# Optimization experiments

Hardware: AMD Instinct MI355X
Metric: run time of the kernel (lower is better)

## Reference

```python
import jax, jax.numpy as jnp
import numpy as np
import math

H, D, DFF = 12, 768, 3072
DH = D // H  # 64
B, T = 4, 2048
EPS = 1e-5


def setup_inputs() -> dict:
    key = jax.random.key(0)
    ks = jax.random.split(key, 12)
    randw = lambda k, *d: jax.random.normal(k, d, jnp.float32) / math.sqrt(d[-1])
    return {
        "X": jax.random.normal(ks[0], (B, T, D), jnp.float32),
        "w_q": randw(ks[1], H, DH, D),
        "w_k": randw(ks[2], H, DH, D),
        "w_v": randw(ks[3], H, DH, D),
        "w_o": randw(ks[4], DH * H, D),
        "W1": jax.random.normal(ks[5], (DFF, D), jnp.float32) * 0.02,
        "b1": jnp.zeros((DFF,), jnp.float32),
        "W2": jax.random.normal(ks[6], (D, DFF), jnp.float32) * 0.02,
        "b2": jnp.zeros((D,), jnp.float32),
        "g1": jnp.ones((D,), jnp.float32),
        "be1": jnp.zeros((D,), jnp.float32),
        "g2": jnp.ones((D,), jnp.float32),
        "be2": jnp.zeros((D,), jnp.float32),
    }


def layernorm(x, g, b):
    mu = jnp.mean(x, axis=-1, keepdims=True)
    var = jnp.var(x, axis=-1, keepdims=True)
    return (x - mu) * jax.lax.rsqrt(var + EPS) * g + b


def attention(x, w_q, w_k, w_v, w_o):
    # x: [n,t,c]
    q = jnp.einsum('ntc,hdc->nhtd', x, w_q)
    k = jnp.einsum('ntc,hdc->nhtd', x, w_k)
    v = jnp.einsum('ntc,hdc->nhtd', x, w_v)
    a = jnp.einsum('nhtd,nhsd->nhts', q, k) / math.sqrt(q.shape[3])
    t, s = a.shape[2], a.shape[3]
    forbidden = jnp.arange(t)[:, None] < jnp.arange(s)[None, :]
    a = jnp.where(forbidden, -jnp.inf, a)
    a = jax.nn.softmax(a, axis=3)
    y = jnp.einsum('nhts,nhsd->nthd', a, v).reshape(x.shape[0], t, -1)
    return y @ w_o


def reference(X, w_q, w_k, w_v, w_o, W1, b1, W2, b2, g1, be1, g2, be2):
    X = X + attention(layernorm(X, g1, be1), w_q, w_k, w_v, w_o)
    h = jax.nn.relu(layernorm(X, g2, be2) @ W1.T + b1)
    return X + h @ W2.T + b2
```

## Files before the change

### kernel.cpp

```cpp
#include <hip/hip_runtime.h>
#include <stdint.h>

#define B_   4
#define T_   2048
#define D_   768
#define H_   12
#define DH_  64
#define DFF_ 3072
#define NTOK_ (B_*T_)
#define QKVN_ (3*D_)

typedef unsigned short u16;
typedef __bf16 bf16x8 __attribute__((ext_vector_type(8)));
typedef float  f32x4  __attribute__((ext_vector_type(4)));

__device__ __forceinline__ u16 f2bf(float f) {
  union { float f; unsigned u; } v; v.f = f;
  return (u16)((v.u + 0x7fffu + ((v.u >> 16) & 1u)) >> 16);
}

__device__ __forceinline__ u16 f2bf_ru(float f) {
  union { float f; unsigned u; } v; v.f = f;
  return (u16)((v.u + 0x8000u) >> 16);
}

__device__ __forceinline__ float fast_exp2(float x) {
#if __has_builtin(__builtin_amdgcn_exp2f)
  return __builtin_amdgcn_exp2f(x);
#else
  return exp2f(x);
#endif
}

__device__ __forceinline__ float fast_rcp(float x) {
#if __has_builtin(__builtin_amdgcn_rcpf)
  return __builtin_amdgcn_rcpf(x);
#else
  return 1.0f / x;
#endif
}

__device__ __forceinline__ void gload_lds16(const void* g, void* l) {
  __builtin_amdgcn_global_load_lds(
      (__attribute__((address_space(1))) unsigned int*)(void*)g,
      (__attribute__((address_space(3))) unsigned int*)l, 16, 0, 0);
}

template<bool BIAS, bool RELU, bool RES, bool BF16OUT, bool QSCALE, int BN>
__global__ __launch_bounds__(256) void gemm_bt(
    const u16* __restrict__ A, const u16* __restrict__ Bw,
    const float* __restrict__ bias, const float* __restrict__ res,
    void* __restrict__ outp, int M, int N, int K)
{
  constexpr int NI = BN / 32;
  __shared__ u16 lA[128 * 32];
  __shared__ u16 lB[BN * 32];
  const int tid  = threadIdx.x;
  const int lane = tid & 63;
  const int wave = tid >> 6;
  const int quad = lane >> 4;
  const int l15  = lane & 15;
  const int mBase = blockIdx.x * 128;
  const int nBase = blockIdx.y * BN;
  const int wm = (wave >> 1) * 64;
  const int wn = (wave & 1) * (BN / 2);

  const f32x4 fz = {0.f, 0.f, 0.f, 0.f};
  f32x4 acc[4][NI];
#pragma unroll
  for (int i = 0; i < 4; i++)
#pragma unroll
    for (int j = 0; j < NI; j++) acc[i][j] = fz;

  const int c0 = tid, c1 = tid + 256;
  const u16* gA0 = A  + (size_t)(mBase + (c0 >> 2)) * K + (c0 & 3) * 8;
  const u16* gA1 = A  + (size_t)(mBase + (c1 >> 2)) * K + (c1 & 3) * 8;
  const u16* gB0 = Bw + (size_t)(nBase + (c0 >> 2)) * K + (c0 & 3) * 8;
  const u16* gB1 = (BN == 128)
      ? Bw + (size_t)(nBase + (c1 >> 2)) * K + (c1 & 3) * 8 : nullptr;
  u16* lA0 = lA + c0 * 8; u16* lA1 = lA + c1 * 8;
  u16* lB0 = lB + c0 * 8;
  u16* lB1 = (BN == 128) ? lB + c1 * 8 : nullptr;

  for (int kt = 0; kt < K; kt += 32) {
    gload_lds16(gA0 + kt, lA0);
    gload_lds16(gA1 + kt, lA1);
    gload_lds16(gB0 + kt, lB0);
    if (BN == 128) gload_lds16(gB1 + kt, lB1);
    __syncthreads();
    bf16x8 af[4], bfr[NI];
#pragma unroll
    for (int mi = 0; mi < 4; mi++)
      af[mi] = *(const bf16x8*)(lA + (wm + mi * 16 + l15) * 32 + quad * 8);
#pragma unroll
    for (int ni = 0; ni < NI; ni++)
      bfr[ni] = *(const bf16x8*)(lB + (wn + ni * 16 + l15) * 32 + quad * 8);
#pragma unroll
    for (int mi = 0; mi < 4; mi++)
#pragma unroll
      for (int ni = 0; ni < NI; ni++)
        acc[mi][ni] = __builtin_amdgcn_mfma_f32_16x16x32_bf16(
            af[mi], bfr[ni], acc[mi][ni], 0, 0, 0);
    __syncthreads();
  }

#pragma unroll
  for (int mi = 0; mi < 4; mi++) {
#pragma unroll
    for (int ni = 0; ni < NI; ni++) {
      const int col = nBase + wn + ni * 16 + l15;
      float bv = 0.f;
      if (BIAS) bv = bias[col];
#pragma unroll
      for (int r = 0; r < 4; r++) {
        const int row = mBase + wm + mi * 16 + quad * 4 + r;
        float v = acc[mi][ni][r];
        if (BIAS) v += bv;
        if (RELU) v = fmaxf(v, 0.f);
        if (RES)  v += res[(size_t)row * N + col];
        if (QSCALE && col < D_) v *= 0.180336880f;
        if (BF16OUT) ((u16*)outp)[(size_t)row * N + col] = f2bf(v);
        else        ((float*)outp)[(size_t)row * N + col] = v;
      }
    }
  }
}

__global__ __launch_bounds__(256) void attn_kernel(
    const u16* __restrict__ qkv, const u16* __restrict__ vt, u16* __restrict__ Y)
{
  __shared__ u16 lK[2][64 * 64];
  __shared__ u16 lV[2][64 * 64];
  __shared__ u16 lP[4][16 * 64];
  const int tid  = threadIdx.x;
  const int lane = tid & 63;
  const int wave = tid >> 6;
  const int quad = lane >> 4;
  const int l15  = lane & 15;
  const int qt = 31 - (int)blockIdx.x;
  const int q0 = qt * 64;
  const int h  = blockIdx.y;
  const int b  = blockIdx.z;
  const int qw = q0 + wave * 16;

  bf16x8 qf0, qf1;
  {
    const u16* qp = qkv + (size_t)(b * T_ + qw + l15) * QKVN_ + h * DH_ + quad * 8;
    qf0 = *(const bf16x8*)(qp);
    qf1 = *(const bf16x8*)(qp + 32);
  }

  const f32x4 fz = {0.f, 0.f, 0.f, 0.f};
  f32x4 o[4];
#pragma unroll
  for (int i = 0; i < 4; i++) o[i] = fz;
  float lsum[4] = {0.f, 0.f, 0.f, 0.f};

  const int c0 = tid, c1 = tid + 256;
  const int r0 = c0 >> 3, j0 = (c0 & 7) ^ (r0 & 7);
  const int r1 = c1 >> 3, j1 = (c1 & 7) ^ (r1 & 7);
  const u16* gK0 = qkv + (size_t)(b * T_ + r0) * QKVN_ + D_ + h * DH_ + j0 * 8;
  const u16* gK1 = qkv + (size_t)(b * T_ + r1) * QKVN_ + D_ + h * DH_ + j1 * 8;
  const u16* gV0 = vt + (size_t)((b * H_ + h) * DH_ + r0) * T_ + j0 * 8;
  const u16* gV1 = vt + (size_t)((b * H_ + h) * DH_ + r1) * T_ + j1 * 8;

  const int njs = qt + 1;

  gload_lds16(gK0, lK[0] + c0 * 8);
  gload_lds16(gK1, lK[0] + c1 * 8);
  gload_lds16(gV0, lV[0] + c0 * 8);
  gload_lds16(gV1, lV[0] + c1 * 8);

  for (int js = 0; js < njs; js++) {
    const int cur = js & 1;
    __syncthreads();

    if (js + 1 < njs) {
      const size_t s1 = (size_t)(js + 1) * 64;
      const int nb = cur ^ 1;
      gload_lds16(gK0 + s1 * QKVN_, lK[nb] + c0 * 8);
      gload_lds16(gK1 + s1 * QKVN_, lK[nb] + c1 * 8);
      gload_lds16(gV0 + s1,         lV[nb] + c0 * 8);
      gload_lds16(gV1 + s1,         lV[nb] + c1 * 8);
    }

    const u16* lKc = lK[cur];
    const u16* lVc = lV[cur];

    f32x4 sa[4];
#pragma unroll
    for (int ni = 0; ni < 4; ni++) {
      const int row = ni * 16 + l15;
      const int sw = row & 7;
      const bf16x8 k0 = *(const bf16x8*)(lKc + row * 64 + ((quad ^ sw) * 8));
      const bf16x8 k1 = *(const bf16x8*)(lKc + row * 64 + (((4 + quad) ^ sw) * 8));
      f32x4 t = fz;
      t = __builtin_amdgcn_mfma_f32_16x16x32_bf16(qf0, k0, t, 0, 0, 0);
      t = __builtin_amdgcn_mfma_f32_16x16x32_bf16(qf1, k1, t, 0, 0, 0);
      sa[ni] = t;
    }

    if (js != qt) {
#pragma unroll
      for (int ni = 0; ni < 4; ni++)
#pragma unroll
        for (int r = 0; r < 4; r++) {
          const float p = fast_exp2(sa[ni][r]);
          sa[ni][r] = p;
          lsum[r] += p;
        }
    } else {
      const int qloc = wave * 16 + quad * 4;
#pragma unroll
      for (int ni = 0; ni < 4; ni++) {
        const int sloc = ni * 16 + l15;
#pragma unroll
        for (int r = 0; r < 4; r++) {
          const float p = (sloc > qloc + r) ? 0.f : fast_exp2(sa[ni][r]);
          sa[ni][r] = p;
          lsum[r] += p;
        }
      }
    }

    u16* lp = lP[wave];
#pragma unroll
    for (int ni = 0; ni < 4; ni++) {
      const int colc = ni * 2 + (l15 >> 3);
      const int cole = l15 & 7;
#pragma unroll
      for (int r = 0; r < 4; r++) {
        const int row = quad * 4 + r;
        lp[row * 64 + ((colc ^ (row & 7)) * 8) + cole] = f2bf_ru(sa[ni][r]);
      }
    }
    __asm__ volatile("s_waitcnt lgkmcnt(0)" ::: "memory");
    const int swp = l15 & 7;
    const bf16x8 p0 = *(const bf16x8*)(lp + l15 * 64 + ((quad ^ swp) * 8));
    const bf16x8 p1 = *(const bf16x8*)(lp + l15 * 64 + (((4 + quad) ^ swp) * 8));
#pragma unroll
    for (int dt = 0; dt < 4; dt++) {
      const int row = dt * 16 + l15;
      const int sw = row & 7;
      const bf16x8 v0 = *(const bf16x8*)(lVc + row * 64 + ((quad ^ sw) * 8));
      const bf16x8 v1 = *(const bf16x8*)(lVc + row * 64 + (((4 + quad) ^ sw) * 8));
      o[dt] = __builtin_amdgcn_mfma_f32_16x16x32_bf16(p0, v0, o[dt], 0, 0, 0);
      o[dt] = __builtin_amdgcn_mfma_f32_16x16x32_bf16(p1, v1, o[dt], 0, 0, 0);
    }
  }

#pragma unroll
  for (int off = 1; off < 16; off <<= 1)
#pragma unroll
    for (int r = 0; r < 4; r++) lsum[r] += __shfl_xor(lsum[r], off);
  float rl[4];
#pragma unroll
  for (int r = 0; r < 4; r++) rl[r] = fast_rcp(lsum[r]);

#pragma unroll
  for (int dt = 0; dt < 4; dt++)
#pragma unroll
    for (int r = 0; r < 4; r++) {
      const int q = qw + quad * 4 + r;
      const int col = h * DH_ + dt * 16 + l15;
      Y[(size_t)(b * T_ + q) * D_ + col] = f2bf(o[dt][r] * rl[r]);
    }
}

__global__ __launch_bounds__(256) void vtrans_kernel(
    const u16* __restrict__ qkv, u16* __restrict__ vt)
{
  __shared__ u16 tile[64][72];
  const int t0 = blockIdx.x * 64;
  const int h = blockIdx.y, b = blockIdx.z;
  for (int idx = threadIdx.x; idx < 4096; idx += 256) {
    const int ts = idx >> 6, d = idx & 63;
    tile[ts][d] = qkv[(size_t)(b * T_ + t0 + ts) * QKVN_ + 2 * D_ + h * DH_ + d];
  }
  __syncthreads();
  for (int idx = threadIdx.x; idx < 4096; idx += 256) {
    const int d = idx >> 6, ts = idx & 63;
    vt[(size_t)((b * H_ + h) * DH_ + d) * T_ + t0 + ts] = tile[ts][d];
  }
}

__global__ __launch_bounds__(256) void ln_kernel(
    const float* __restrict__ X, const float* __restrict__ g,
    const float* __restrict__ be, u16* __restrict__ out)
{
  const int row = blockIdx.x;
  const float* x = X + (size_t)row * D_;
  const int t = threadIdx.x;
  const float v0 = x[t], v1 = x[t + 256], v2 = x[t + 512];
  float s = v0 + v1 + v2;
  float sq = v0 * v0 + v1 * v1 + v2 * v2;
#pragma unroll
  for (int off = 1; off < 64; off <<= 1) {
    s  += __shfl_xor(s, off);
    sq += __shfl_xor(sq, off);
  }
  __shared__ float ws_[4], wq_[4];
  const int wv = t >> 6, lane = t & 63;
  if (lane == 0) { ws_[wv] = s; wq_[wv] = sq; }
  __syncthreads();
  s  = ws_[0] + ws_[1] + ws_[2] + ws_[3];
  sq = wq_[0] + wq_[1] + wq_[2] + wq_[3];
  const float mean = s * (1.f / 768.f);
  const float var  = sq * (1.f / 768.f) - mean * mean;
  const float rstd = rsqrtf(var + 1e-5f);
  u16* o = out + (size_t)row * D_;
  int c = t;
  o[c] = f2bf((v0 - mean) * rstd * g[c] + be[c]); c += 256;
  o[c] = f2bf((v1 - mean) * rstd * g[c] + be[c]); c += 256;
  o[c] = f2bf((v2 - mean) * rstd * g[c] + be[c]);
}

__global__ __launch_bounds__(256) void wcvt_kernel(
    const float* __restrict__ w_q, const float* __restrict__ w_k,
    const float* __restrict__ w_v, const float* __restrict__ W1,
    const float* __restrict__ W2, const float* __restrict__ w_o,
    u16* __restrict__ wqkv, u16* __restrict__ W1b,
    u16* __restrict__ W2b, u16* __restrict__ woT)
{
  const int id = blockIdx.x;
  if (id < 144) {
    __shared__ float tile[64][65];
    const int bx = id % 12, by = id / 12;
    const int rr0 = by * 64, cc0 = bx * 64;
    for (int idx = threadIdx.x; idx < 4096; idx += 256) {
      const int i = idx >> 6, j = idx & 63;
      tile[i][j] = w_o[(size_t)(rr0 + i) * D_ + cc0 + j];
    }
    __syncthreads();
    for (int idx = threadIdx.x; idx < 4096; idx += 256) {
      const int i = idx >> 6, j = idx & 63;
      woT[(size_t)(cc0 + i) * D_ + rr0 + j] = f2bf(tile[j][i]);
    }
  } else {
    const int WQN = H_ * DH_ * D_;
    const int i = (id - 144) * 256 + threadIdx.x;
    if (i < 3 * WQN) {
      const float* src = (i < WQN) ? w_q : (i < 2 * WQN ? w_k : w_v);
      const int off = (i < WQN) ? i : (i < 2 * WQN ? i - WQN : i - 2 * WQN);
      wqkv[i] = f2bf(src[off]);
    } else if (i < 3 * WQN + DFF_ * D_) {
      const int off = i - 3 * WQN;
      W1b[off] = f2bf(W1[off]);
    } else {
      const int off = i - 3 * WQN - DFF_ * D_;
      W2b[off] = f2bf(W2[off]);
    }
  }
}

extern "C" void kernel_launch(void* const* d_in, const int* in_sizes, int n_in,
                              void* d_out, int out_size, void* d_ws, size_t ws_size,
                              hipStream_t stream) {
  const float* X   = (const float*)d_in[0];
  const float* w_q = (const float*)d_in[1];
  const float* w_k = (const float*)d_in[2];
  const float* w_v = (const float*)d_in[3];
  const float* w_o = (const float*)d_in[4];
  const float* W1  = (const float*)d_in[5];
  const float* b1  = (const float*)d_in[6];
  const float* W2  = (const float*)d_in[7];
  const float* b2  = (const float*)d_in[8];
  const float* g1  = (const float*)d_in[9];
  const float* be1 = (const float*)d_in[10];
  const float* g2  = (const float*)d_in[11];
  const float* be2 = (const float*)d_in[12];
  float* out = (float*)d_out;

  char* ws = (char*)d_ws;
  u16*   qkv  = (u16*)(ws + 0);
  u16*   vt   = (u16*)(ws + 37748736);
  u16*   hbuf = (u16*)(ws + 0);
  u16*   xln  = (u16*)(ws + 50331648);
  u16*   Ybuf = (u16*)(ws + 62914560);
  float* X1   = (float*)(ws + 75497472);
  u16*   wqkv = (u16*)(ws + 100663296);
  u16*   woT  = (u16*)(ws + 104202240);
  u16*   W1b  = (u16*)(ws + 105381888);
  u16*   W2b  = (u16*)(ws + 110100480);

  wcvt_kernel<<<25488, 256, 0, stream>>>(w_q, w_k, w_v, W1, W2, w_o,
                                         wqkv, W1b, W2b, woT);

  ln_kernel<<<NTOK_, 256, 0, stream>>>(X, g1, be1, xln);

  gemm_bt<false, false, false, true, true, 128><<<dim3(64, 18), 256, 0, stream>>>(
      xln, wqkv, nullptr, nullptr, qkv, NTOK_, QKVN_, D_);

  vtrans_kernel<<<dim3(32, 12, 4), 256, 0, stream>>>(qkv, vt);
  attn_kernel<<<dim3(32, 12, 4), 256, 0, stream>>>(qkv, vt, Ybuf);

  gemm_bt<false, false, true, false, false, 64><<<dim3(64, 12), 256, 0, stream>>>(
      Ybuf, woT, nullptr, X, X1, NTOK_, D_, D_);

  ln_kernel<<<NTOK_, 256, 0, stream>>>(X1, g2, be2, xln);

  gemm_bt<true, true, false, true, false, 128><<<dim3(64, 24), 256, 0, stream>>>(
      xln, W1b, b1, nullptr, hbuf, NTOK_, DFF_, D_);

  gemm_bt<true, false, true, false, false, 64><<<dim3(64, 12), 256, 0, stream>>>(
      hbuf, W2b, b2, X1, out, NTOK_, D_, DFF_);
}
```

Measured before the change: 415.5 us.

## Fuse V transpose into QKV GEMM, merge prep kernels, deepen GEMM K-step

The QKV GEMM epilogue now writes the V columns straight into the transposed vt layout, so the separate vtrans kernel goes away. The first layernorm and the weight conversion are merged into one prep launch. The GEMM main loop loads 64 K-elements per barrier pair using doubled LDS buffers, halving the number of syncs. The attention kernel loads its V fragments before the softmax so LDS latency can overlap it. Together these aim to cut launch count and memory round trips, at the cost of more LDS use per block and a strided 8-byte scatter for the vt stores.

```diff
diff --git a/kernel.cpp b/kernel.cpp
--- a/kernel.cpp
+++ b/kernel.cpp
@@ -46,15 +46,16 @@
       (__attribute__((address_space(3))) unsigned int*)l, 16, 0, 0);
 }
 
-template<bool BIAS, bool RELU, bool RES, bool BF16OUT, bool QSCALE, int BN>
+template<bool BIAS, bool RELU, bool RES, bool BF16OUT, bool QSCALE, int BN,
+         bool VTRANS>
 __global__ __launch_bounds__(256) void gemm_bt(
     const u16* __restrict__ A, const u16* __restrict__ Bw,
     const float* __restrict__ bias, const float* __restrict__ res,
-    void* __restrict__ outp, int M, int N, int K)
+    void* __restrict__ outp, u16* __restrict__ vtp, int M, int N, int K)
 {
   constexpr int NI = BN / 32;
-  __shared__ u16 lA[128 * 32];
-  __shared__ u16 lB[BN * 32];
+  __shared__ u16 lA[2 * 128 * 32];
+  __shared__ u16 lB[2 * BN * 32];
   const int tid  = threadIdx.x;
   const int lane = tid & 63;
   const int wave = tid >> 6;
@@ -82,25 +83,36 @@
   u16* lB0 = lB + c0 * 8;
   u16* lB1 = (BN == 128) ? lB + c1 * 8 : nullptr;
 
-  for (int kt = 0; kt < K; kt += 32) {
-    gload_lds16(gA0 + kt, lA0);
-    gload_lds16(gA1 + kt, lA1);
-    gload_lds16(gB0 + kt, lB0);
-    if (BN == 128) gload_lds16(gB1 + kt, lB1);
+  for (int kt = 0; kt < K; kt += 64) {
+    gload_lds16(gA0 + kt,      lA0);
+    gload_lds16(gA1 + kt,      lA1);
+    gload_lds16(gA0 + kt + 32, lA0 + 128 * 32);
+    gload_lds16(gA1 + kt + 32, lA1 + 128 * 32);
+    gload_lds16(gB0 + kt,      lB0);
+    gload_lds16(gB0 + kt + 32, lB0 + BN * 32);
+    if (BN == 128) {
+      gload_lds16(gB1 + kt,      lB1);
+      gload_lds16(gB1 + kt + 32, lB1 + BN * 32);
+    }
     __syncthreads();
-    bf16x8 af[4], bfr[NI];
-#pragma unroll
-    for (int mi = 0; mi < 4; mi++)
-      af[mi] = *(const bf16x8*)(lA + (wm + mi * 16 + l15) * 32 + quad * 8);
-#pragma unroll
-    for (int ni = 0; ni < NI; ni++)
-      bfr[ni] = *(const bf16x8*)(lB + (wn + ni * 16 + l15) * 32 + quad * 8);
-#pragma unroll
-    for (int mi = 0; mi < 4; mi++)
+#pragma unroll
+    for (int hf = 0; hf < 2; hf++) {
+      const u16* lAh = lA + hf * (128 * 32);
+      const u16* lBh = lB + hf * (BN * 32);
+      bf16x8 af[4], bfr[NI];
+#pragma unroll
+      for (int mi = 0; mi < 4; mi++)
+        af[mi] = *(const bf16x8*)(lAh + (wm + mi * 16 + l15) * 32 + quad * 8);
 #pragma unroll
       for (int ni = 0; ni < NI; ni++)
-        acc[mi][ni] = __builtin_amdgcn_mfma_f32_16x16x32_bf16(
-            af[mi], bfr[ni], acc[mi][ni], 0, 0, 0);
+        bfr[ni] = *(const bf16x8*)(lBh + (wn + ni * 16 + l15) * 32 + quad * 8);
+#pragma unroll
+      for (int mi = 0; mi < 4; mi++)
+#pragma unroll
+        for (int ni = 0; ni < NI; ni++)
+          acc[mi][ni] = __builtin_amdgcn_mfma_f32_16x16x32_bf16(
+              af[mi], bfr[ni], acc[mi][ni], 0, 0, 0);
+    }
     __syncthreads();
   }
 
@@ -109,6 +121,17 @@
 #pragma unroll
     for (int ni = 0; ni < NI; ni++) {
       const int col = nBase + wn + ni * 16 + l15;
+      if (VTRANS && col >= 2 * D_) {
+        const int n  = col - 2 * D_;
+        const int hh = n >> 6, dd = n & 63;
+        const int row0 = mBase + wm + mi * 16 + quad * 4;
+        const int bb = row0 >> 11, tt = row0 & (T_ - 1);
+        ushort4 pk;
+        pk.x = f2bf(acc[mi][ni][0]); pk.y = f2bf(acc[mi][ni][1]);
+        pk.z = f2bf(acc[mi][ni][2]); pk.w = f2bf(acc[mi][ni][3]);
+        *(ushort4*)(vtp + ((size_t)((bb * H_ + hh) * DH_ + dd)) * T_ + tt) = pk;
+        continue;
+      }
       float bv = 0.f;
       if (BIAS) bv = bias[col];
 #pragma unroll
@@ -200,6 +223,15 @@
       sa[ni] = t;
     }
 
+    bf16x8 vf0[4], vf1[4];
+#pragma unroll
+    for (int dt = 0; dt < 4; dt++) {
+      const int row = dt * 16 + l15;
+      const int sw = row & 7;
+      vf0[dt] = *(const bf16x8*)(lVc + row * 64 + ((quad ^ sw) * 8));
+      vf1[dt] = *(const bf16x8*)(lVc + row * 64 + (((4 + quad) ^ sw) * 8));
+    }
+
     if (js != qt) {
 #pragma unroll
       for (int ni = 0; ni < 4; ni++)
@@ -240,12 +272,8 @@
     const bf16x8 p1 = *(const bf16x8*)(lp + l15 * 64 + (((4 + quad) ^ swp) * 8));
 #pragma unroll
     for (int dt = 0; dt < 4; dt++) {
-      const int row = dt * 16 + l15;
-      const int sw = row & 7;
-      const bf16x8 v0 = *(const bf16x8*)(lVc + row * 64 + ((quad ^ sw) * 8));
-      const bf16x8 v1 = *(const bf16x8*)(lVc + row * 64 + (((4 + quad) ^ sw) * 8));
-      o[dt] = __builtin_amdgcn_mfma_f32_16x16x32_bf16(p0, v0, o[dt], 0, 0, 0);
-      o[dt] = __builtin_amdgcn_mfma_f32_16x16x32_bf16(p1, v1, o[dt], 0, 0, 0);
+      o[dt] = __builtin_amdgcn_mfma_f32_16x16x32_bf16(p0, vf0[dt], o[dt], 0, 0, 0);
+      o[dt] = __builtin_amdgcn_mfma_f32_16x16x32_bf16(p1, vf1[dt], o[dt], 0, 0, 0);
     }
   }
 
@@ -267,28 +295,10 @@
     }
 }
 
-__global__ __launch_bounds__(256) void vtrans_kernel(
-    const u16* __restrict__ qkv, u16* __restrict__ vt)
+__device__ __forceinline__ void ln_row(
+    const float* __restrict__ X, const float* __restrict__ g,
+    const float* __restrict__ be, u16* __restrict__ out, int row)
 {
-  __shared__ u16 tile[64][72];
-  const int t0 = blockIdx.x * 64;
-  const int h = blockIdx.y, b = blockIdx.z;
-  for (int idx = threadIdx.x; idx < 4096; idx += 256) {
-    const int ts = idx >> 6, d = idx & 63;
-    tile[ts][d] = qkv[(size_t)(b * T_ + t0 + ts) * QKVN_ + 2 * D_ + h * DH_ + d];
-  }
-  __syncthreads();
-  for (int idx = threadIdx.x; idx < 4096; idx += 256) {
-    const int d = idx >> 6, ts = idx & 63;
-    vt[(size_t)((b * H_ + h) * DH_ + d) * T_ + t0 + ts] = tile[ts][d];
-  }
-}
-
-__global__ __launch_bounds__(256) void ln_kernel(
-    const float* __restrict__ X, const float* __restrict__ g,
-    const float* __restrict__ be, u16* __restrict__ out)
-{
-  const int row = blockIdx.x;
   const float* x = X + (size_t)row * D_;
   const int t = threadIdx.x;
   const float v0 = x[t], v1 = x[t + 256], v2 = x[t + 512];
@@ -315,14 +325,27 @@
   o[c] = f2bf((v2 - mean) * rstd * g[c] + be[c]);
 }
 
-__global__ __launch_bounds__(256) void wcvt_kernel(
+__global__ __launch_bounds__(256) void ln_kernel(
+    const float* __restrict__ X, const float* __restrict__ g,
+    const float* __restrict__ be, u16* __restrict__ out)
+{
+  ln_row(X, g, be, out, blockIdx.x);
+}
+
+__global__ __launch_bounds__(256) void prep_kernel(
+    const float* __restrict__ X, const float* __restrict__ g1,
+    const float* __restrict__ be1, u16* __restrict__ xln,
     const float* __restrict__ w_q, const float* __restrict__ w_k,
     const float* __restrict__ w_v, const float* __restrict__ W1,
     const float* __restrict__ W2, const float* __restrict__ w_o,
     u16* __restrict__ wqkv, u16* __restrict__ W1b,
     u16* __restrict__ W2b, u16* __restrict__ woT)
 {
-  const int id = blockIdx.x;
+  if (blockIdx.x < NTOK_) {
+    ln_row(X, g1, be1, xln, blockIdx.x);
+    return;
+  }
+  const int id = blockIdx.x - NTOK_;
   if (id < 144) {
     __shared__ float tile[64][65];
     const int bx = id % 12, by = id / 12;
@@ -383,25 +406,26 @@
   u16*   W1b  = (u16*)(ws + 105381888);
   u16*   W2b  = (u16*)(ws + 110100480);
 
-  wcvt_kernel<<<25488, 256, 0, stream>>>(w_q, w_k, w_v, W1, W2, w_o,
-                                         wqkv, W1b, W2b, woT);
-
-  ln_kernel<<<NTOK_, 256, 0, stream>>>(X, g1, be1, xln);
-
-  gemm_bt<false, false, false, true, true, 128><<<dim3(64, 18), 256, 0, stream>>>(
-      xln, wqkv, nullptr, nullptr, qkv, NTOK_, QKVN_, D_);
-
-  vtrans_kernel<<<dim3(32, 12, 4), 256, 0, stream>>>(qkv, vt);
+  prep_kernel<<<NTOK_ + 25488, 256, 0, stream>>>(
+      X, g1, be1, xln, w_q, w_k, w_v, W1, W2, w_o, wqkv, W1b, W2b, woT);
+
+  gemm_bt<false, false, false, true, true, 128, true>
+      <<<dim3(64, 18), 256, 0, stream>>>(
+      xln, wqkv, nullptr, nullptr, qkv, vt, NTOK_, QKVN_, D_);
+
   attn_kernel<<<dim3(32, 12, 4), 256, 0, stream>>>(qkv, vt, Ybuf);
 
-  gemm_bt<false, false, true, false, false, 64><<<dim3(64, 12), 256, 0, stream>>>(
-      Ybuf, woT, nullptr, X, X1, NTOK_, D_, D_);
+  gemm_bt<false, false, true, false, false, 64, false>
+      <<<dim3(64, 12), 256, 0, stream>>>(
+      Ybuf, woT, nullptr, X, X1, nullptr, NTOK_, D_, D_);
 
   ln_kernel<<<NTOK_, 256, 0, stream>>>(X1, g2, be2, xln);
 
-  gemm_bt<true, true, false, true, false, 128><<<dim3(64, 24), 256, 0, stream>>>(
-      xln, W1b, b1, nullptr, hbuf, NTOK_, DFF_, D_);
-
-  gemm_bt<true, false, true, false, false, 64><<<dim3(64, 12), 256, 0, stream>>>(
-      hbuf, W2b, b2, X1, out, NTOK_, D_, DFF_);
-}
+  gemm_bt<true, true, false, true, false, 128, false>
+      <<<dim3(64, 24), 256, 0, stream>>>(
+      xln, W1b, b1, nullptr, hbuf, nullptr, NTOK_, DFF_, D_);
+
+  gemm_bt<true, false, true, false, false, 64, false>
+      <<<dim3(64, 12), 256, 0, stream>>>(
+      hbuf, W2b, b2, X1, out, nullptr, NTOK_, D_, DFF_);
+}
```

After: 388.7 us. 6.5% less time.
